# Kernel optimization log

Measured on AMD Instinct MI355X. Metric: run time of the kernel, lower is better.

Reference implementation:

```python
import jax, jax.numpy as jnp
import numpy as np

N, D, H = 500000, 128, 128
B, M = 1024, 512


def setup_inputs() -> dict:
    key = jax.random.key(0)
    k = jax.random.split(key, 8)
    return {
        "embed": jax.random.normal(k[0], (N, D), dtype=jnp.float32),
        "node_feat": jax.random.normal(k[1], (N, D), dtype=jnp.float32),
        "W1": jax.random.normal(k[2], (2 * D, H), dtype=jnp.float32) * 0.05,
        "b1": jnp.zeros((H,), dtype=jnp.float32),
        "W2": jax.random.normal(k[3], (H, 1), dtype=jnp.float32) * 0.05,
        "b2": jnp.zeros((1,), dtype=jnp.float32),
        "query_idx": jax.random.randint(k[4], (B,), 0, N),
        "cand_idx": jax.random.randint(k[5], (B, M), 0, N),
        "top_k": 3,
    }


def reference(embed, node_feat, W1, b1, W2, b2, query_idx, cand_idx, top_k):
    # Gather query and candidate (k-hop subgraph) embeddings.
    q = embed[query_idx]                                   # [B, D]
    c = embed[cand_idx]                                    # [B, M, D]
    Bv, Mv, Dv = c.shape
    pair = jnp.concatenate(
        [jnp.broadcast_to(q[:, None, :], (Bv, Mv, Dv)), c], axis=-1
    )                                                      # [B, M, 2D]
    # Tiny 2-layer MLP edge scorer (one fused pass over all edges).
    h = jax.nn.relu(jnp.einsum("bmf,fh->bmh", pair, W1) + b1)
    scores = (jnp.einsum("bmh,ho->bmo", h, W2) + b2)[..., 0]  # [B, M]
    # Sort-based top-k selection (original sorted per-etype lists).
    _, pos = jax.lax.top_k(scores, top_k)                  # [B, k]
    top_nodes = jnp.take_along_axis(cand_idx, pos, axis=1) # [B, k]
    # Zero out features of the selected nodes (hard mask), as in original.
    masked_feat = node_feat.at[top_nodes.reshape(-1)].set(0.0)
    return scores, masked_feat
```

## Files before the change

kernel.cpp:

```cpp
#include <hip/hip_runtime.h>
#include <math.h>

#define D 128
#define H 128
#define BQ 1024
#define M 512
#define NNODES 500000
#define K_MAX 8
#define SHORT 16
#define NCOPYP 1536
#define NSCORE (BQ * 2)
#define COPY_N4 ((long)NNODES * D / 4)
#define CSTRIDE ((long)NCOPYP * 256)

typedef __attribute__((ext_vector_type(8))) short bf16x8;
typedef __attribute__((ext_vector_type(4))) float f32x4;
typedef __attribute__((ext_vector_type(4))) unsigned u32x4;

static __device__ __forceinline__ unsigned pack2bf(float a, float b) {
    unsigned ua = __float_as_uint(a);
    unsigned ub = __float_as_uint(b);
    ua = ua + 0x7fffu + ((ua >> 16) & 1u);
    ub = ub + 0x7fffu + ((ub >> 16) & 1u);
    return (ua >> 16) | (ub & 0xffff0000u);
}

__global__ void wconv_kernel(const float* __restrict__ W1,
                             unsigned short* __restrict__ wTswz) {
    const int idx = blockIdx.x * 256 + threadIdx.x;
    const int h = idx >> 7;
    const int inner = (idx & 127) * 2;
    const int k = (inner ^ ((h & 15) << 4)) >> 1;
    const float v = W1[(long)(D + k) * H + h];
    wTswz[idx] = (unsigned short)pack2bf(v, 0.f);
}

__global__ void qproj_kernel(const float* __restrict__ embed,
                             const float* __restrict__ W1,
                             const float* __restrict__ b1,
                             const int* __restrict__ query_idx,
                             float* __restrict__ qh) {
    __shared__ float qrow[D];
    const int b = blockIdx.x;
    const int t = threadIdx.x;
    const long qi = query_idx[b];
    qrow[t] = embed[qi * D + t];
    __syncthreads();
    float acc = b1[t];
#pragma unroll 8
    for (int d = 0; d < D; ++d)
        acc = fmaf(qrow[d], W1[d * H + t], acc);
    qh[b * H + t] = acc;
}

__global__ __launch_bounds__(256, 4)
void fused_kernel(const float* __restrict__ embed,
                  const unsigned short* __restrict__ wTswz,
                  const float* __restrict__ W2,
                  const float* __restrict__ b2,
                  const int* __restrict__ cand_idx,
                  const float* __restrict__ qh,
                  float* __restrict__ scores,
                  const f32x4* __restrict__ nf_src,
                  f32x4* __restrict__ nf_dst) {
    __shared__ __align__(16) char Bs[32768];
    const int bid = blockIdx.x;
    const int t   = threadIdx.x;

    if (bid < NCOPYP) {
        long i = (long)bid * 256 + t;
        for (; i + 3 * CSTRIDE < COPY_N4; i += 4 * CSTRIDE) {
            const f32x4 v0 = __builtin_nontemporal_load(&nf_src[i]);
            const f32x4 v1 = __builtin_nontemporal_load(&nf_src[i + CSTRIDE]);
            const f32x4 v2 = __builtin_nontemporal_load(&nf_src[i + 2 * CSTRIDE]);
            const f32x4 v3 = __builtin_nontemporal_load(&nf_src[i + 3 * CSTRIDE]);
            __builtin_nontemporal_store(v0, &nf_dst[i]);
            __builtin_nontemporal_store(v1, &nf_dst[i + CSTRIDE]);
            __builtin_nontemporal_store(v2, &nf_dst[i + 2 * CSTRIDE]);
            __builtin_nontemporal_store(v3, &nf_dst[i + 3 * CSTRIDE]);
        }
        for (; i < COPY_N4; i += CSTRIDE) {
            const f32x4 v = __builtin_nontemporal_load(&nf_src[i]);
            __builtin_nontemporal_store(v, &nf_dst[i]);
        }
        return;
    }

    const int sid  = bid - NCOPYP;
    const int b    = sid >> 1;
    const int half = sid & 1;

    {
#pragma unroll
        for (int i = 0; i < 8; ++i) {
            const int c = i * 256 + t;
            const uint4 v = ((const uint4*)wTswz)[c];
            *(uint4*)(Bs + (size_t)c * 16) = v;
        }
    }

    const int lane = t & 63;
    const int w    = t >> 6;
    const int g    = lane >> 4;
    const int c    = lane & 15;
    const int sw   = c << 4;

    float qv[8], w2[8];
#pragma unroll
    for (int cb = 0; cb < 8; ++cb) {
        qv[cb] = qh[b * H + cb * 16 + c];
        w2[cb] = W2[cb * 16 + c];
    }
    const float b2v = b2[0];

    int idx[4];
    const int ibase = b * M + half * 256 + w * 16 + c;
#pragma unroll
    for (int mt = 0; mt < 4; ++mt) idx[mt] = cand_idx[ibase + mt * 64];

    __syncthreads();

    f32x4 buf[8];
    {
        const float* rp = embed + (long)idx[0] * D + g * 8;
#pragma unroll
        for (int ks = 0; ks < 4; ++ks) {
            buf[2 * ks]     = *(const f32x4*)(rp + ks * 32);
            buf[2 * ks + 1] = *(const f32x4*)(rp + ks * 32 + 4);
        }
    }

#pragma unroll
    for (int mt = 0; mt < 4; ++mt) {
        bf16x8 afr[4];
#pragma unroll
        for (int ks = 0; ks < 4; ++ks) {
            u32x4 u;
            u.x = pack2bf(buf[2 * ks].x, buf[2 * ks].y);
            u.y = pack2bf(buf[2 * ks].z, buf[2 * ks].w);
            u.z = pack2bf(buf[2 * ks + 1].x, buf[2 * ks + 1].y);
            u.w = pack2bf(buf[2 * ks + 1].z, buf[2 * ks + 1].w);
            afr[ks] = __builtin_bit_cast(bf16x8, u);
        }
        if (mt < 3) {
            const float* rp = embed + (long)idx[mt + 1] * D + g * 8;
#pragma unroll
            for (int ks = 0; ks < 4; ++ks) {
                buf[2 * ks]     = *(const f32x4*)(rp + ks * 32);
                buf[2 * ks + 1] = *(const f32x4*)(rp + ks * 32 + 4);
            }
        }

        f32x4 acc[8];
#pragma unroll
        for (int cb = 0; cb < 8; ++cb) acc[cb] = (f32x4){0.f, 0.f, 0.f, 0.f};
#pragma unroll
        for (int ks = 0; ks < 4; ++ks) {
            const int koff = (ks * 64 + g * 16) ^ sw;
#pragma unroll
            for (int cb = 0; cb < 8; ++cb) {
                const bf16x8 bv = *(const bf16x8*)(Bs + ((cb * 16 + c) << 8) + koff);
                acc[cb] = __builtin_amdgcn_mfma_f32_16x16x32_bf16(afr[ks], bv, acc[cb], 0, 0, 0);
            }
        }

        float s0 = 0.f, s1 = 0.f, s2 = 0.f, s3 = 0.f;
#pragma unroll
        for (int cb = 0; cb < 8; ++cb) {
            s0 = fmaf(fmaxf(qv[cb] + acc[cb][0], 0.f), w2[cb], s0);
            s1 = fmaf(fmaxf(qv[cb] + acc[cb][1], 0.f), w2[cb], s1);
            s2 = fmaf(fmaxf(qv[cb] + acc[cb][2], 0.f), w2[cb], s2);
            s3 = fmaf(fmaxf(qv[cb] + acc[cb][3], 0.f), w2[cb], s3);
        }
#pragma unroll
        for (int off = 1; off <= 8; off <<= 1) {
            s0 += __shfl_xor(s0, off);
            s1 += __shfl_xor(s1, off);
            s2 += __shfl_xor(s2, off);
            s3 += __shfl_xor(s3, off);
        }
        if (c == 0) {
            float* out = scores + b * M + half * 256 + mt * 64 + w * 16 + g * 4;
            out[0] = s0 + b2v;
            out[1] = s1 + b2v;
            out[2] = s2 + b2v;
            out[3] = s3 + b2v;
        }
    }
}

__global__ void topk16_kernel(const float* __restrict__ scores,
                              int* __restrict__ shortpos) {
    const int b = blockIdx.x;
    const int lane = threadIdx.x;
    const float* row = scores + b * M;
    float v[8];
    {
        const float4 x0 = ((const float4*)row)[lane * 2];
        const float4 x1 = ((const float4*)row)[lane * 2 + 1];
        v[0] = x0.x; v[1] = x0.y; v[2] = x0.z; v[3] = x0.w;
        v[4] = x1.x; v[5] = x1.y; v[6] = x1.z; v[7] = x1.w;
    }
    for (int kk = 0; kk < SHORT; ++kk) {
        float bv = v[0];
        int bi = lane * 8;
#pragma unroll
        for (int j = 1; j < 8; ++j)
            if (v[j] > bv) { bv = v[j]; bi = lane * 8 + j; }
#pragma unroll
        for (int off = 32; off >= 1; off >>= 1) {
            const float ov = __shfl_xor(bv, off);
            const int   oi = __shfl_xor(bi, off);
            if (ov > bv || (ov == bv && oi < bi)) { bv = ov; bi = oi; }
        }
        if (lane == 0) shortpos[b * SHORT + kk] = bi;
        if ((bi >> 3) == lane) v[bi & 7] = -3.402823466e38f;
    }
}

__global__ __launch_bounds__(128)
void refine_kernel(const float* __restrict__ embed,
                   const float* __restrict__ W1,
                   const float* __restrict__ W2,
                   const float* __restrict__ qh,
                   const int* __restrict__ cand_idx,
                   const int* __restrict__ shortpos,
                   const int* __restrict__ topk_ptr,
                   int* __restrict__ top_nodes) {
    __shared__ float crows[SHORT][D];
    __shared__ float red[SHORT][D];
    __shared__ int spos[SHORT];
    const int b = blockIdx.x;
    const int t = threadIdx.x;

    if (t < SHORT) spos[t] = shortpos[b * SHORT + t];
    __syncthreads();
    {
        const int cc = t >> 3;
        const int d0 = (t & 7) * 16;
        const long node = cand_idx[b * M + spos[cc]];
        const float4* rp = (const float4*)(embed + node * D);
        float4* wp = (float4*)&crows[cc][d0];
#pragma unroll
        for (int j = 0; j < 4; ++j) wp[j] = rp[d0 / 4 + j];
    }
    __syncthreads();

    float acc[SHORT];
#pragma unroll
    for (int cc = 0; cc < SHORT; ++cc) acc[cc] = 0.f;
    const float* W1bot = W1 + (long)D * H;
    for (int d = 0; d < D; ++d) {
        const float w1v = W1bot[d * H + t];
#pragma unroll
        for (int cc = 0; cc < SHORT; ++cc)
            acc[cc] = fmaf(crows[cc][d], w1v, acc[cc]);
    }
    const float qv = qh[b * H + t];
    const float w2 = W2[t];
#pragma unroll
    for (int cc = 0; cc < SHORT; ++cc)
        red[cc][t] = fmaxf(qv + acc[cc], 0.f) * w2;
    __syncthreads();

    if (t < 64) {
#pragma unroll
        for (int cc = 0; cc < SHORT; ++cc) {
            float v = red[cc][t] + red[cc][t + 64];
#pragma unroll
            for (int off = 32; off >= 1; off >>= 1) v += __shfl_xor(v, off);
            if (t == 0) red[cc][0] = v;
        }
    }
    __syncthreads();

    if (t == 0) {
        int k = *topk_ptr;
        if (k > K_MAX) k = K_MAX;
        unsigned used = 0;
        for (int kk = 0; kk < K_MAX; ++kk) {
            if (kk < k) {
                int best = -1, bpos = 0x7fffffff;
                float bv = 0.f;
                for (int cc = 0; cc < SHORT; ++cc) {
                    if (used & (1u << cc)) continue;
                    const float v = red[cc][0];
                    const int p = spos[cc];
                    if (best < 0 || v > bv || (v == bv && p < bpos)) {
                        best = cc; bv = v; bpos = p;
                    }
                }
                used |= 1u << best;
                top_nodes[b * K_MAX + kk] = cand_idx[b * M + bpos];
            } else {
                top_nodes[b * K_MAX + kk] = -1;
            }
        }
    }
}

__global__ void zero_rows_kernel(const int* __restrict__ top_nodes,
                                 float* __restrict__ masked) {
    const int node = top_nodes[blockIdx.x];
    if (node < 0) return;
    masked[(long)node * D + threadIdx.x] = 0.f;
}

extern "C" void kernel_launch(void* const* d_in, const int* in_sizes, int n_in,
                              void* d_out, int out_size, void* d_ws, size_t ws_size,
                              hipStream_t stream) {
    const float* embed     = (const float*)d_in[0];
    const float* node_feat = (const float*)d_in[1];
    const float* W1        = (const float*)d_in[2];
    const float* b1        = (const float*)d_in[3];
    const float* W2        = (const float*)d_in[4];
    const float* b2        = (const float*)d_in[5];
    const int*   query_idx = (const int*)d_in[6];
    const int*   cand_idx  = (const int*)d_in[7];
    const int*   topk_ptr  = (const int*)d_in[8];

    float* scores = (float*)d_out;
    float* masked = (float*)d_out + (long)BQ * M;

    char* p = (char*)d_ws;
    float*          qh        = (float*)p;          p += (long)BQ * H * 4;
    int*            shortpos  = (int*)p;            p += (long)BQ * SHORT * 4;
    int*            top_nodes = (int*)p;            p += (long)BQ * K_MAX * 4;
    unsigned short* wTswz     = (unsigned short*)p;

    wconv_kernel<<<(H * D) / 256, 256, 0, stream>>>(W1, wTswz);
    qproj_kernel<<<BQ, H, 0, stream>>>(embed, W1, b1, query_idx, qh);

    fused_kernel<<<NCOPYP + NSCORE, 256, 0, stream>>>(
        embed, wTswz, W2, b2, cand_idx, qh, scores,
        (const f32x4*)node_feat, (f32x4*)masked);

    topk16_kernel<<<BQ, 64, 0, stream>>>(scores, shortpos);
    refine_kernel<<<BQ, 128, 0, stream>>>(embed, W1, W2, qh, cand_idx,
                                          shortpos, topk_ptr, top_nodes);
    zero_rows_kernel<<<BQ * K_MAX, D, 0, stream>>>(top_nodes, masked);
}
```

Baseline: 188.3 us.

## Interleave node_feat copy into scoring blocks instead of separate copy blocks

Removes the dedicated copy blocks and has every scoring block copy its own strided share of node_feat, with loads and stores interleaved around the gather and MFMA phases of each tile. The aim is to hide the bulk copy's memory traffic behind the scoring work and to avoid imbalance between the two kinds of block. The cost is higher register pressure and longer-running blocks, which may hurt occupancy at the launch bound of 4.

```diff
diff --git a/kernel.cpp b/kernel.cpp
--- a/kernel.cpp
+++ b/kernel.cpp
@@ -8,10 +8,9 @@
 #define NNODES 500000
 #define K_MAX 8
 #define SHORT 16
-#define NCOPYP 1536
-#define NSCORE (BQ * 2)
+#define NBLK 2048
 #define COPY_N4 ((long)NNODES * D / 4)
-#define CSTRIDE ((long)NCOPYP * 256)
+#define CS ((long)NBLK * 256)
 
 typedef __attribute__((ext_vector_type(8))) short bf16x8;
 typedef __attribute__((ext_vector_type(4))) float f32x4;
@@ -67,28 +66,9 @@
     const int bid = blockIdx.x;
     const int t   = threadIdx.x;
 
-    if (bid < NCOPYP) {
-        long i = (long)bid * 256 + t;
-        for (; i + 3 * CSTRIDE < COPY_N4; i += 4 * CSTRIDE) {
-            const f32x4 v0 = __builtin_nontemporal_load(&nf_src[i]);
-            const f32x4 v1 = __builtin_nontemporal_load(&nf_src[i + CSTRIDE]);
-            const f32x4 v2 = __builtin_nontemporal_load(&nf_src[i + 2 * CSTRIDE]);
-            const f32x4 v3 = __builtin_nontemporal_load(&nf_src[i + 3 * CSTRIDE]);
-            __builtin_nontemporal_store(v0, &nf_dst[i]);
-            __builtin_nontemporal_store(v1, &nf_dst[i + CSTRIDE]);
-            __builtin_nontemporal_store(v2, &nf_dst[i + 2 * CSTRIDE]);
-            __builtin_nontemporal_store(v3, &nf_dst[i + 3 * CSTRIDE]);
-        }
-        for (; i < COPY_N4; i += CSTRIDE) {
-            const f32x4 v = __builtin_nontemporal_load(&nf_src[i]);
-            __builtin_nontemporal_store(v, &nf_dst[i]);
-        }
-        return;
-    }
-
-    const int sid  = bid - NCOPYP;
-    const int b    = sid >> 1;
-    const int half = sid & 1;
+    const int b    = bid >> 1;
+    const int half = bid & 1;
+    const long cbase = (long)bid * 256 + t;
 
     {
 #pragma unroll
@@ -132,6 +112,13 @@
 
 #pragma unroll
     for (int mt = 0; mt < 4; ++mt) {
+        f32x4 ca[4];
+#pragma unroll
+        for (int j = 0; j < 4; ++j) {
+            const long i = cbase + (long)(mt * 8 + j) * CS;
+            if (i < COPY_N4) ca[j] = __builtin_nontemporal_load(&nf_src[i]);
+        }
+
         bf16x8 afr[4];
 #pragma unroll
         for (int ks = 0; ks < 4; ++ks) {
@@ -151,6 +138,18 @@
             }
         }
 
+#pragma unroll
+        for (int j = 0; j < 4; ++j) {
+            const long i = cbase + (long)(mt * 8 + j) * CS;
+            if (i < COPY_N4) __builtin_nontemporal_store(ca[j], &nf_dst[i]);
+        }
+        f32x4 cbv[4];
+#pragma unroll
+        for (int j = 0; j < 4; ++j) {
+            const long i = cbase + (long)(mt * 8 + 4 + j) * CS;
+            if (i < COPY_N4) cbv[j] = __builtin_nontemporal_load(&nf_src[i]);
+        }
+
         f32x4 acc[8];
 #pragma unroll
         for (int cb = 0; cb < 8; ++cb) acc[cb] = (f32x4){0.f, 0.f, 0.f, 0.f};
@@ -179,6 +178,13 @@
             s2 += __shfl_xor(s2, off);
             s3 += __shfl_xor(s3, off);
         }
+
+#pragma unroll
+        for (int j = 0; j < 4; ++j) {
+            const long i = cbase + (long)(mt * 8 + 4 + j) * CS;
+            if (i < COPY_N4) __builtin_nontemporal_store(cbv[j], &nf_dst[i]);
+        }
+
         if (c == 0) {
             float* out = scores + b * M + half * 256 + mt * 64 + w * 16 + g * 4;
             out[0] = s0 + b2v;
@@ -331,7 +337,7 @@
     wconv_kernel<<<(H * D) / 256, 256, 0, stream>>>(W1, wTswz);
     qproj_kernel<<<BQ, H, 0, stream>>>(embed, W1, b1, query_idx, qh);
 
-    fused_kernel<<<NCOPYP + NSCORE, 256, 0, stream>>>(
+    fused_kernel<<<NBLK, 256, 0, stream>>>(
         embed, wTswz, W2, b2, cand_idx, qh, scores,
         (const f32x4*)node_feat, (f32x4*)masked);
 
```

After: 256.8 us. 36.4% more time.

## Fuse small kernels and switch the scoring/copy kernel to 512-thread blocks

Applied to the files above, without the earlier changes.

Merges the weight-conversion and query-projection kernels into one pre-kernel, and merges the top-16 shortlist, refine and row-zeroing kernels into a single per-query kernel, cutting launches from six to three. The fused scoring kernel now uses 512-thread blocks that each cover a whole query row, and the copy partition changes from 1536 to 1024 blocks. The aim is less launch and inter-kernel overhead and fewer redundant weight loads into shared memory. Zeroing rows inside the per-query kernel means duplicate top nodes across queries are written concurrently by different blocks, which is harmless because every write stores zero.

```diff
diff --git a/kernel.cpp b/kernel.cpp
--- a/kernel.cpp
+++ b/kernel.cpp
@@ -8,10 +8,10 @@
 #define NNODES 500000
 #define K_MAX 8
 #define SHORT 16
-#define NCOPYP 1536
-#define NSCORE (BQ * 2)
+#define NCOPYP 1024
+#define NSCORE 1024
 #define COPY_N4 ((long)NNODES * D / 4)
-#define CSTRIDE ((long)NCOPYP * 256)
+#define CS ((long)NCOPYP * 512)
 
 typedef __attribute__((ext_vector_type(8))) short bf16x8;
 typedef __attribute__((ext_vector_type(4))) float f32x4;
@@ -25,24 +25,25 @@
     return (ua >> 16) | (ub & 0xffff0000u);
 }
 
-__global__ void wconv_kernel(const float* __restrict__ W1,
-                             unsigned short* __restrict__ wTswz) {
-    const int idx = blockIdx.x * 256 + threadIdx.x;
-    const int h = idx >> 7;
-    const int inner = (idx & 127) * 2;
-    const int k = (inner ^ ((h & 15) << 4)) >> 1;
-    const float v = W1[(long)(D + k) * H + h];
-    wTswz[idx] = (unsigned short)pack2bf(v, 0.f);
-}
-
-__global__ void qproj_kernel(const float* __restrict__ embed,
-                             const float* __restrict__ W1,
-                             const float* __restrict__ b1,
-                             const int* __restrict__ query_idx,
-                             float* __restrict__ qh) {
+__global__ __launch_bounds__(128)
+void pre_kernel(const float* __restrict__ embed,
+                const float* __restrict__ W1,
+                const float* __restrict__ b1,
+                const int* __restrict__ query_idx,
+                float* __restrict__ qh,
+                unsigned short* __restrict__ wTswz) {
     __shared__ float qrow[D];
     const int b = blockIdx.x;
     const int t = threadIdx.x;
+
+    if (b < 128) {
+        const int idx = b * 128 + t;
+        const int h = idx >> 7;
+        const int inner = (idx & 127) * 2;
+        const int k = (inner ^ ((h & 15) << 4)) >> 1;
+        wTswz[idx] = (unsigned short)pack2bf(W1[(long)(D + k) * H + h], 0.f);
+    }
+
     const long qi = query_idx[b];
     qrow[t] = embed[qi * D + t];
     __syncthreads();
@@ -53,7 +54,7 @@
     qh[b * H + t] = acc;
 }
 
-__global__ __launch_bounds__(256, 4)
+__global__ __launch_bounds__(512, 8)
 void fused_kernel(const float* __restrict__ embed,
                   const unsigned short* __restrict__ wTswz,
                   const float* __restrict__ W2,
@@ -68,32 +69,30 @@
     const int t   = threadIdx.x;
 
     if (bid < NCOPYP) {
-        long i = (long)bid * 256 + t;
-        for (; i + 3 * CSTRIDE < COPY_N4; i += 4 * CSTRIDE) {
+        long i = (long)bid * 512 + t;
+        for (; i + 3 * CS < COPY_N4; i += 4 * CS) {
             const f32x4 v0 = __builtin_nontemporal_load(&nf_src[i]);
-            const f32x4 v1 = __builtin_nontemporal_load(&nf_src[i + CSTRIDE]);
-            const f32x4 v2 = __builtin_nontemporal_load(&nf_src[i + 2 * CSTRIDE]);
-            const f32x4 v3 = __builtin_nontemporal_load(&nf_src[i + 3 * CSTRIDE]);
+            const f32x4 v1 = __builtin_nontemporal_load(&nf_src[i + CS]);
+            const f32x4 v2 = __builtin_nontemporal_load(&nf_src[i + 2 * CS]);
+            const f32x4 v3 = __builtin_nontemporal_load(&nf_src[i + 3 * CS]);
             __builtin_nontemporal_store(v0, &nf_dst[i]);
-            __builtin_nontemporal_store(v1, &nf_dst[i + CSTRIDE]);
-            __builtin_nontemporal_store(v2, &nf_dst[i + 2 * CSTRIDE]);
-            __builtin_nontemporal_store(v3, &nf_dst[i + 3 * CSTRIDE]);
-        }
-        for (; i < COPY_N4; i += CSTRIDE) {
+            __builtin_nontemporal_store(v1, &nf_dst[i + CS]);
+            __builtin_nontemporal_store(v2, &nf_dst[i + 2 * CS]);
+            __builtin_nontemporal_store(v3, &nf_dst[i + 3 * CS]);
+        }
+        for (; i < COPY_N4; i += CS) {
             const f32x4 v = __builtin_nontemporal_load(&nf_src[i]);
             __builtin_nontemporal_store(v, &nf_dst[i]);
         }
         return;
     }
 
-    const int sid  = bid - NCOPYP;
-    const int b    = sid >> 1;
-    const int half = sid & 1;
+    const int b = bid - NCOPYP;
 
     {
 #pragma unroll
-        for (int i = 0; i < 8; ++i) {
-            const int c = i * 256 + t;
+        for (int i = 0; i < 4; ++i) {
+            const int c = i * 512 + t;
             const uint4 v = ((const uint4*)wTswz)[c];
             *(uint4*)(Bs + (size_t)c * 16) = v;
         }
@@ -101,6 +100,8 @@
 
     const int lane = t & 63;
     const int w    = t >> 6;
+    const int band = w & 3;
+    const int hf   = w >> 2;
     const int g    = lane >> 4;
     const int c    = lane & 15;
     const int sw   = c << 4;
@@ -114,7 +115,7 @@
     const float b2v = b2[0];
 
     int idx[4];
-    const int ibase = b * M + half * 256 + w * 16 + c;
+    const int ibase = b * M + hf * 256 + band * 16 + c;
 #pragma unroll
     for (int mt = 0; mt < 4; ++mt) idx[mt] = cand_idx[ibase + mt * 64];
 
@@ -180,7 +181,7 @@
             s3 += __shfl_xor(s3, off);
         }
         if (c == 0) {
-            float* out = scores + b * M + half * 256 + mt * 64 + w * 16 + g * 4;
+            float* out = scores + b * M + hf * 256 + mt * 64 + band * 16 + g * 4;
             out[0] = s0 + b2v;
             out[1] = s1 + b2v;
             out[2] = s2 + b2v;
@@ -189,52 +190,48 @@
     }
 }
 
-__global__ void topk16_kernel(const float* __restrict__ scores,
-                              int* __restrict__ shortpos) {
-    const int b = blockIdx.x;
-    const int lane = threadIdx.x;
-    const float* row = scores + b * M;
-    float v[8];
-    {
-        const float4 x0 = ((const float4*)row)[lane * 2];
-        const float4 x1 = ((const float4*)row)[lane * 2 + 1];
-        v[0] = x0.x; v[1] = x0.y; v[2] = x0.z; v[3] = x0.w;
-        v[4] = x1.x; v[5] = x1.y; v[6] = x1.z; v[7] = x1.w;
-    }
-    for (int kk = 0; kk < SHORT; ++kk) {
-        float bv = v[0];
-        int bi = lane * 8;
-#pragma unroll
-        for (int j = 1; j < 8; ++j)
-            if (v[j] > bv) { bv = v[j]; bi = lane * 8 + j; }
-#pragma unroll
-        for (int off = 32; off >= 1; off >>= 1) {
-            const float ov = __shfl_xor(bv, off);
-            const int   oi = __shfl_xor(bi, off);
-            if (ov > bv || (ov == bv && oi < bi)) { bv = ov; bi = oi; }
-        }
-        if (lane == 0) shortpos[b * SHORT + kk] = bi;
-        if ((bi >> 3) == lane) v[bi & 7] = -3.402823466e38f;
-    }
-}
-
 __global__ __launch_bounds__(128)
-void refine_kernel(const float* __restrict__ embed,
-                   const float* __restrict__ W1,
-                   const float* __restrict__ W2,
-                   const float* __restrict__ qh,
-                   const int* __restrict__ cand_idx,
-                   const int* __restrict__ shortpos,
-                   const int* __restrict__ topk_ptr,
-                   int* __restrict__ top_nodes) {
+void topkrefine_kernel(const float* __restrict__ embed,
+                       const float* __restrict__ W1,
+                       const float* __restrict__ W2,
+                       const float* __restrict__ qh,
+                       const int* __restrict__ cand_idx,
+                       const float* __restrict__ scores,
+                       const int* __restrict__ topk_ptr,
+                       float* __restrict__ masked) {
     __shared__ float crows[SHORT][D];
     __shared__ float red[SHORT][D];
     __shared__ int spos[SHORT];
+    __shared__ int tnodes[K_MAX];
+    __shared__ int kshare;
     const int b = blockIdx.x;
     const int t = threadIdx.x;
 
-    if (t < SHORT) spos[t] = shortpos[b * SHORT + t];
-    __syncthreads();
+    if (t < 64) {
+        const float* row = scores + b * M;
+        float v[8];
+        const float4 x0 = ((const float4*)row)[t * 2];
+        const float4 x1 = ((const float4*)row)[t * 2 + 1];
+        v[0] = x0.x; v[1] = x0.y; v[2] = x0.z; v[3] = x0.w;
+        v[4] = x1.x; v[5] = x1.y; v[6] = x1.z; v[7] = x1.w;
+        for (int kk = 0; kk < SHORT; ++kk) {
+            float bv = v[0];
+            int bi = t * 8;
+#pragma unroll
+            for (int j = 1; j < 8; ++j)
+                if (v[j] > bv) { bv = v[j]; bi = t * 8 + j; }
+#pragma unroll
+            for (int off = 32; off >= 1; off >>= 1) {
+                const float ov = __shfl_xor(bv, off);
+                const int   oi = __shfl_xor(bi, off);
+                if (ov > bv || (ov == bv && oi < bi)) { bv = ov; bi = oi; }
+            }
+            if (t == 0) spos[kk] = bi;
+            if ((bi >> 3) == t) v[bi & 7] = -3.402823466e38f;
+        }
+    }
+    __syncthreads();
+
     {
         const int cc = t >> 3;
         const int d0 = (t & 7) * 16;
@@ -277,33 +274,27 @@
     if (t == 0) {
         int k = *topk_ptr;
         if (k > K_MAX) k = K_MAX;
+        kshare = k;
         unsigned used = 0;
-        for (int kk = 0; kk < K_MAX; ++kk) {
-            if (kk < k) {
-                int best = -1, bpos = 0x7fffffff;
-                float bv = 0.f;
-                for (int cc = 0; cc < SHORT; ++cc) {
-                    if (used & (1u << cc)) continue;
-                    const float v = red[cc][0];
-                    const int p = spos[cc];
-                    if (best < 0 || v > bv || (v == bv && p < bpos)) {
-                        best = cc; bv = v; bpos = p;
-                    }
+        for (int kk = 0; kk < k; ++kk) {
+            int best = -1, bpos = 0x7fffffff;
+            float bv = 0.f;
+            for (int cc = 0; cc < SHORT; ++cc) {
+                if (used & (1u << cc)) continue;
+                const float v = red[cc][0];
+                const int p = spos[cc];
+                if (best < 0 || v > bv || (v == bv && p < bpos)) {
+                    best = cc; bv = v; bpos = p;
                 }
-                used |= 1u << best;
-                top_nodes[b * K_MAX + kk] = cand_idx[b * M + bpos];
-            } else {
-                top_nodes[b * K_MAX + kk] = -1;
             }
-        }
-    }
-}
-
-__global__ void zero_rows_kernel(const int* __restrict__ top_nodes,
-                                 float* __restrict__ masked) {
-    const int node = top_nodes[blockIdx.x];
-    if (node < 0) return;
-    masked[(long)node * D + threadIdx.x] = 0.f;
+            used |= 1u << best;
+            tnodes[kk] = cand_idx[b * M + bpos];
+        }
+    }
+    __syncthreads();
+
+    for (int kk = 0; kk < kshare; ++kk)
+        masked[(long)tnodes[kk] * D + t] = 0.f;
 }
 
 extern "C" void kernel_launch(void* const* d_in, const int* in_sizes, int n_in,
@@ -323,20 +314,15 @@
     float* masked = (float*)d_out + (long)BQ * M;
 
     char* p = (char*)d_ws;
-    float*          qh        = (float*)p;          p += (long)BQ * H * 4;
-    int*            shortpos  = (int*)p;            p += (long)BQ * SHORT * 4;
-    int*            top_nodes = (int*)p;            p += (long)BQ * K_MAX * 4;
-    unsigned short* wTswz     = (unsigned short*)p;
-
-    wconv_kernel<<<(H * D) / 256, 256, 0, stream>>>(W1, wTswz);
-    qproj_kernel<<<BQ, H, 0, stream>>>(embed, W1, b1, query_idx, qh);
-
-    fused_kernel<<<NCOPYP + NSCORE, 256, 0, stream>>>(
+    float*          qh    = (float*)p;              p += (long)BQ * H * 4;
+    unsigned short* wTswz = (unsigned short*)p;
+
+    pre_kernel<<<BQ, 128, 0, stream>>>(embed, W1, b1, query_idx, qh, wTswz);
+
+    fused_kernel<<<NCOPYP + NSCORE, 512, 0, stream>>>(
         embed, wTswz, W2, b2, cand_idx, qh, scores,
         (const f32x4*)node_feat, (f32x4*)masked);
 
-    topk16_kernel<<<BQ, 64, 0, stream>>>(scores, shortpos);
-    refine_kernel<<<BQ, 128, 0, stream>>>(embed, W1, W2, qh, cand_idx,
-                                          shortpos, topk_ptr, top_nodes);
-    zero_rows_kernel<<<BQ * K_MAX, D, 0, stream>>>(top_nodes, masked);
-}
+    topkrefine_kernel<<<BQ, 128, 0, stream>>>(embed, W1, W2, qh, cand_idx,
+                                              scores, topk_ptr, masked);
+}
```

Result: slower. 239.1 us (+27.0%).
